# Performance work log

Measured on AMD Instinct MI355X. Metric: run time of the kernel, lower is better.

## Reference

```python
import jax, jax.numpy as jnp
import numpy as np

B, N, DIN, D, PHI, RHO, L = 4096, 10, 32, 128, 256, 128, 3
EPS = 1e-5


def setup_inputs() -> dict:
    key = jax.random.key(0)
    ks = jax.random.split(key, 24)
    def p(k, shape):
        return jax.random.normal(k, shape, jnp.float32) * 0.05
    return {
        "A": jax.random.normal(ks[0], (B, N, N), jnp.float32),
        "X": jax.random.normal(ks[1], (B, N, DIN), jnp.float32),
        "home_mask": jax.random.randint(ks[2], (B, N), 0, 2).astype(jnp.int32),
        "We1": p(ks[3], (DIN, D)), "be1": p(ks[4], (D,)),
        "We2": p(ks[5], (D, D)), "be2": p(ks[6], (D,)),
        "rgcn_w": p(ks[7], (L, 2, D, D)),      # per-relation weights
        "rgcn_root": p(ks[8], (L, D, D)),       # root (self) weight
        "rgcn_b": p(ks[9], (L, D)),
        "l1w": p(ks[10], (L, D, D)), "l1b": p(ks[11], (L, D)),
        "l2w": p(ks[12], (L, D, D)), "l2b": p(ks[13], (L, D)),
        "ln_g": jnp.ones((D,), jnp.float32), "ln_b": jnp.zeros((D,), jnp.float32),
        "p1w": p(ks[14], (D, PHI)), "p1b": p(ks[15], (PHI,)),
        "p2w": p(ks[16], (PHI, PHI)), "p2b": p(ks[17], (PHI,)),
        "r1w": p(ks[18], (PHI, RHO)), "r1b": p(ks[19], (RHO,)),
        "r2w": p(ks[20], (RHO, 1)), "r2b": p(ks[21], (1,)),
    }


def _layernorm(x, g, b):
    mu = x.mean(-1, keepdims=True)
    var = ((x - mu) ** 2).mean(-1, keepdims=True)
    return (x - mu) / jnp.sqrt(var + EPS) * g + b


def reference(A, X, home_mask, We1, be1, We2, be2, rgcn_w, rgcn_root, rgcn_b,
              l1w, l1b, l2w, l2b, ln_g, ln_b, p1w, p1b, p2w, p2b,
              r1w, r1b, r2w, r2b):
    BN = B * N
    hm = home_mask.astype(jnp.float32)
    am = 1.0 - hm
    # embedders (dropout layers are identity in eval)
    H = jax.nn.relu(X @ We1 + be1)
    H = (H @ We2 + be2).reshape(BN, D)
    # A ~ randn is nonzero everywhere -> edge list = all (b,i,j) pairs,
    # in the same row-major order torch.nonzero produces.
    bidx = jnp.repeat(jnp.arange(BN), N)          # b*N+i for each edge (row)
    row = bidx
    col = (jnp.repeat(jnp.arange(B), N * N) * N + jnp.tile(jnp.arange(N), BN))
    ew = A.reshape(-1)                             # edge weight
    aw = jnp.abs(ew)
    m1 = (ew > 0).astype(jnp.float32)              # relation 1 mask
    m0 = 1.0 - m1                                  # relation 0 mask
    agg = jnp.zeros_like(H)
    for l in range(L):
        H = H + agg
        # RGCNConv (mean aggregation per relation + root + bias)
        xj = H[row]                                # [E, D] gather of sources
        s0 = jax.ops.segment_sum(xj * m0[:, None], col, num_segments=BN)
        s1 = jax.ops.segment_sum(xj * m1[:, None], col, num_segments=BN)
        c0 = jax.ops.segment_sum(m0, col, num_segments=BN)
        c1 = jax.ops.segment_sum(m1, col, num_segments=BN)
        mean0 = s0 / jnp.maximum(c0, 1.0)[:, None]
        mean1 = s1 / jnp.maximum(c1, 1.0)[:, None]
        H2 = mean0 @ rgcn_w[l, 0] + mean1 @ rgcn_w[l, 1] + H @ rgcn_root[l] + rgcn_b[l]
        # outer gather-scale-scatter
        msg = H2[col] * aw[:, None]                # [E, D]
        agg = jax.ops.segment_sum(msg, row, num_segments=BN)
        agg = jax.nn.relu(_layernorm(agg, ln_g, ln_b))
        # Linear -> ReLU -> (Dropout=id) -> Linear
        agg = jax.nn.relu(agg @ l1w[l] + l1b[l])
        agg = agg @ l2w[l] + l2b[l]
    H = (H + agg).reshape(B, N, D)
    # DeepSet phi (dropout = identity)
    phi = jax.nn.relu(H @ p1w + p1b)
    phi = jax.nn.relu(phi @ p2w + p2b)             # [B, N, PHI]
    hs = (phi * hm[..., None]).sum(axis=1)
    aws = (phi * am[..., None]).sum(axis=1)
    def rho(s):
        return (jax.nn.relu(s @ r1w + r1b) @ r2w + r2b)[..., 0]
    return 0.5 + 0.5 * jnp.tanh(rho(hs) - rho(aws))
```

## Files before the change

kernel.cpp:

```cpp
#include <hip/hip_runtime.h>
#include <math.h>

#define B_    4096
#define N_    10
#define DIN_  32
#define D_    128
#define PHI_  256
#define RHO_  128
#define L_    3
#define EPS_  1e-5f

__device__ __forceinline__ short f2bs(float f) {
    unsigned u = __float_as_uint(f);
    u += 0x7fffu + ((u >> 16) & 1u);
    return (short)(u >> 16);
}
__device__ __forceinline__ float bs2f(short s) {
    return __uint_as_float(((unsigned)(unsigned short)s) << 16);
}

typedef short bf16x8 __attribute__((ext_vector_type(8)));
typedef float f32x4  __attribute__((ext_vector_type(4)));
typedef float v2f    __attribute__((ext_vector_type(2)));

__device__ __forceinline__ v2f splat2(float s) { v2f r; r.x = s; r.y = s; return r; }
__device__ __forceinline__ v2f fma2(v2f a, v2f b, v2f c) { return __builtin_elementwise_fma(a, b, c); }

#define WS_WE1 0
#define WS_WE2 4096
#define WS_RGW 20480
#define WS_RGR 118784
#define WS_L1  167936
#define WS_L2  217088
#define WS_P1  266240
#define WS_P2  299008
#define WS_R1  364544

__global__ __launch_bounds__(64)
void prep_weights(const float* __restrict__ We1, const float* __restrict__ We2,
                  const float* __restrict__ rgw, const float* __restrict__ rgr,
                  const float* __restrict__ l1w, const float* __restrict__ l2w,
                  const float* __restrict__ p1w, const float* __restrict__ p2w,
                  const float* __restrict__ r1w, short* __restrict__ ws)
{
    int bi = blockIdx.x, l = threadIdx.x;
    const float* src; int KS, Nw, dstOff, tt;
    if      (bi <   8) { src = We1; KS = 1; Nw = 128; dstOff = WS_WE1; tt = bi; }
    else if (bi <  40) { src = We2; KS = 4; Nw = 128; dstOff = WS_WE2; tt = bi - 8; }
    else if (bi < 232) { int m = (bi - 40) >> 5;  src = rgw + m * 16384; KS = 4; Nw = 128; dstOff = WS_RGW + m * 16384; tt = (bi - 40)  & 31; }
    else if (bi < 328) { int m = (bi - 232) >> 5; src = rgr + m * 16384; KS = 4; Nw = 128; dstOff = WS_RGR + m * 16384; tt = (bi - 232) & 31; }
    else if (bi < 424) { int m = (bi - 328) >> 5; src = l1w + m * 16384; KS = 4; Nw = 128; dstOff = WS_L1  + m * 16384; tt = (bi - 328) & 31; }
    else if (bi < 520) { int m = (bi - 424) >> 5; src = l2w + m * 16384; KS = 4; Nw = 128; dstOff = WS_L2  + m * 16384; tt = (bi - 424) & 31; }
    else if (bi < 584) { src = p1w; KS = 4; Nw = 256; dstOff = WS_P1; tt = bi - 520; }
    else if (bi < 712) { src = p2w; KS = 8; Nw = 256; dstOff = WS_P2; tt = bi - 584; }
    else               { src = r1w; KS = 8; Nw = 128; dstOff = WS_R1; tt = bi - 712; }
    int nt = tt / KS, ks = tt - nt * KS;
    int kbase = ks * 32 + (l >> 4) * 8;
    int col   = nt * 16 + (l & 15);
    union { short s[8]; int4 v; } u;
#pragma unroll
    for (int j = 0; j < 8; ++j)
        u.s[j] = f2bs(src[(size_t)(kbase + j) * Nw + col]);
    *(int4*)(ws + dstOff + ((size_t)tt * 64 + l) * 8) = u.v;
}


template<int NT>
__device__ __forceinline__ void initC(f32x4* acc, const float* __restrict__ bias, int c16) {
#pragma unroll
    for (int nt = 0; nt < NT; ++nt) {
        float bv = bias[nt * 16 + c16];
        acc[nt] = (f32x4){bv, bv, bv, bv};
    }
}

template<int KS, int NT>
__device__ __forceinline__ void mm_a16(const short* __restrict__ Wf, const short* __restrict__ Ab,
                                       int ldA, int mrow, int q, int l, f32x4* acc) {
#pragma unroll
    for (int ks = 0; ks < KS; ++ks) {
        bf16x8 a = *(const bf16x8*)(Ab + mrow * ldA + ks * 32 + q * 8);
#pragma unroll
        for (int nt = 0; nt < NT; ++nt) {
            bf16x8 bv = *(const bf16x8*)(Wf + ((size_t)(nt * KS + ks) * 64 + l) * 8);
            acc[nt] = __builtin_amdgcn_mfma_f32_16x16x32_bf16(a, bv, acc[nt], 0, 0, 0);
        }
    }
}

template<int KS, int NT>
__device__ __forceinline__ void mm_a32(const short* __restrict__ Wf, const float* __restrict__ Af,
                                       int ldA, int mrow, int q, int l, f32x4* acc) {
#pragma unroll
    for (int ks = 0; ks < KS; ++ks) {
        const float* p = Af + mrow * ldA + ks * 32 + q * 8;
        f32x4 x0 = *(const f32x4*)p;
        f32x4 x1 = *(const f32x4*)(p + 4);
        bf16x8 a;
        a[0] = f2bs(x0[0]); a[1] = f2bs(x0[1]); a[2] = f2bs(x0[2]); a[3] = f2bs(x0[3]);
        a[4] = f2bs(x1[0]); a[5] = f2bs(x1[1]); a[6] = f2bs(x1[2]); a[7] = f2bs(x1[3]);
#pragma unroll
        for (int nt = 0; nt < NT; ++nt) {
            bf16x8 bv = *(const bf16x8*)(Wf + ((size_t)(nt * KS + ks) * 64 + l) * 8);
            acc[nt] = __builtin_amdgcn_mfma_f32_16x16x32_bf16(a, bv, acc[nt], 0, 0, 0);
        }
    }
}

template<int KS>
__device__ __forceinline__ void mm8p_a16(const short* __restrict__ Wf,
                                         const short* __restrict__ Ab, int ldA,
                                         int mrow, int q, int l, f32x4* acc)
{
    const short* ap = Ab + mrow * ldA + q * 8;
    const short* wp = Wf + l * 8;
    bf16x8 acur = *(const bf16x8*)ap;
    bf16x8 bcur[8], bnxt[8];
#pragma unroll
    for (int nt = 0; nt < 8; ++nt) bcur[nt] = *(const bf16x8*)(wp + (size_t)nt * KS * 512);
#pragma unroll
    for (int ks = 0; ks < KS; ++ks) {
        bf16x8 anxt = acur;
#pragma unroll
        for (int nt = 0; nt < 8; ++nt) bnxt[nt] = bcur[nt];
        if (ks + 1 < KS) {
            anxt = *(const bf16x8*)(ap + (ks + 1) * 32);
#pragma unroll
            for (int nt = 0; nt < 8; ++nt)
                bnxt[nt] = *(const bf16x8*)(wp + (size_t)(nt * KS + ks + 1) * 512);
        }
#pragma unroll
        for (int nt = 0; nt < 8; ++nt)
            acc[nt] = __builtin_amdgcn_mfma_f32_16x16x32_bf16(acur, bcur[nt], acc[nt], 0, 0, 0);
        acur = anxt;
#pragma unroll
        for (int nt = 0; nt < 8; ++nt) bcur[nt] = bnxt[nt];
    }
}

template<int KS>
__device__ __forceinline__ void mm8p_a32(const short* __restrict__ Wf,
                                         const float* __restrict__ Af, int ldA,
                                         int mrow, int q, int l, f32x4* acc)
{
    const float* ap = Af + mrow * ldA + q * 8;
    const short* wp = Wf + l * 8;
    auto cvt = [&](int ks) {
        f32x4 x0 = *(const f32x4*)(ap + ks * 32);
        f32x4 x1 = *(const f32x4*)(ap + ks * 32 + 4);
        bf16x8 a;
        a[0] = f2bs(x0[0]); a[1] = f2bs(x0[1]); a[2] = f2bs(x0[2]); a[3] = f2bs(x0[3]);
        a[4] = f2bs(x1[0]); a[5] = f2bs(x1[1]); a[6] = f2bs(x1[2]); a[7] = f2bs(x1[3]);
        return a;
    };
    bf16x8 acur = cvt(0);
    bf16x8 bcur[8], bnxt[8];
#pragma unroll
    for (int nt = 0; nt < 8; ++nt) bcur[nt] = *(const bf16x8*)(wp + (size_t)nt * KS * 512);
#pragma unroll
    for (int ks = 0; ks < KS; ++ks) {
        bf16x8 anxt = acur;
#pragma unroll
        for (int nt = 0; nt < 8; ++nt) bnxt[nt] = bcur[nt];
        if (ks + 1 < KS) {
            anxt = cvt(ks + 1);
#pragma unroll
            for (int nt = 0; nt < 8; ++nt)
                bnxt[nt] = *(const bf16x8*)(wp + (size_t)(nt * KS + ks + 1) * 512);
        }
#pragma unroll
        for (int nt = 0; nt < 8; ++nt)
            acc[nt] = __builtin_amdgcn_mfma_f32_16x16x32_bf16(acur, bcur[nt], acc[nt], 0, 0, 0);
        acur = anxt;
#pragma unroll
        for (int nt = 0; nt < 8; ++nt) bcur[nt] = bnxt[nt];
    }
}

template<int NT, bool RELU>
__device__ __forceinline__ void storeC16(const f32x4* acc, short* __restrict__ dst,
                                         int ldD, int q, int c16) {
#pragma unroll
    for (int nt = 0; nt < NT; ++nt) {
#pragma unroll
        for (int i = 0; i < 4; ++i) {
            int r = q * 4 + i;
            if (r < 10) {
                float v = acc[nt][i];
                if (RELU) v = fmaxf(v, 0.f);
                dst[r * ldD + nt * 16 + c16] = f2bs(v);
            }
        }
    }
}

#define HLD  132
#define GLD  264
#define H2LD 136

__global__ __launch_bounds__(64, 2)
void gcn_main(const float* __restrict__ A, const float* __restrict__ X,
              const int* __restrict__ home_mask,
              const float* __restrict__ be1, const float* __restrict__ be2,
              const float* __restrict__ rgcn_b,
              const float* __restrict__ l1b, const float* __restrict__ l2b,
              const float* __restrict__ ln_g, const float* __restrict__ ln_b,
              const float* __restrict__ p1b, const float* __restrict__ p2b,
              const float* __restrict__ r1b, const float* __restrict__ r2w,
              const short* __restrict__ ws, float* __restrict__ out)
{
    const int b   = blockIdx.x;
    const int l   = threadIdx.x;
    const int q   = l >> 4;
    const int c16 = l & 15;
    const int mrow = (c16 < 10) ? c16 : 9;

    __shared__ __align__(16) float HfS[N_ * HLD];
    __shared__ __align__(16) short GbS[N_ * GLD];
    __shared__ __align__(16) short H2S[N_ * H2LD];
    __shared__ float AabsS[100], M1S[100];
    __shared__ float invc0S[N_], invc1S[N_];
    __shared__ float hmfS[16], awfS[16];

    short* S0 = GbS;
    short* S1 = GbS + 136;
    short* RhoS = H2S;

    {
        const float* Ab = A + (size_t)b * 100;
#pragma unroll
        for (int e = l; e < 100; e += 64) {
            float a = Ab[e];
            AabsS[e] = fabsf(a);
            M1S[e]  = (a > 0.f) ? 1.f : 0.f;
        }
        if (l < 16) {
            float hm = 0.f, aw = 0.f;
            if (l < 10) { hm = (float)home_mask[b * N_ + l]; aw = 1.f - hm; }
            hmfS[l] = hm; awfS[l] = aw;
        }
        if (l < 10) {
            float c1 = 0.f;
#pragma unroll
            for (int i = 0; i < 10; ++i) c1 += M1S[i * 10 + l];
            invc1S[l] = 1.f / fmaxf(c1, 1.f);
            invc0S[l] = 1.f / fmaxf(10.f - c1, 1.f);
        }
    }

    {
        f32x4 acc[8];
        initC<8>(acc, be1, c16);
        const float* xg = X + (size_t)b * (N_ * DIN_) + mrow * DIN_ + q * 8;
        f32x4 x0 = *(const f32x4*)xg;
        f32x4 x1 = *(const f32x4*)(xg + 4);
        bf16x8 a;
        a[0] = f2bs(x0[0]); a[1] = f2bs(x0[1]); a[2] = f2bs(x0[2]); a[3] = f2bs(x0[3]);
        a[4] = f2bs(x1[0]); a[5] = f2bs(x1[1]); a[6] = f2bs(x1[2]); a[7] = f2bs(x1[3]);
#pragma unroll
        for (int nt = 0; nt < 8; ++nt) {
            bf16x8 bv = *(const bf16x8*)(ws + WS_WE1 + ((size_t)nt * 64 + l) * 8);
            acc[nt] = __builtin_amdgcn_mfma_f32_16x16x32_bf16(a, bv, acc[nt], 0, 0, 0);
        }
        storeC16<8, true>(acc, S0, GLD, q, c16);
    }
    {
        f32x4 acc[8];
        initC<8>(acc, be2, c16);
        mm8p_a16<4>(ws + WS_WE2, S0, GLD, mrow, q, l, acc);
#pragma unroll
        for (int nt = 0; nt < 8; ++nt)
#pragma unroll
            for (int i = 0; i < 4; ++i) {
                int r = q * 4 + i;
                if (r < 10) HfS[r * HLD + nt * 16 + c16] = acc[nt][i];
            }
    }

    const v2f lg2 = *(const v2f*)(ln_g + 2 * l);
    const v2f lb2 = *(const v2f*)(ln_b + 2 * l);

    for (int ll = 0; ll < L_; ++ll) {
        {
            v2f hv[N_];
#pragma unroll
            for (int i = 0; i < N_; ++i) hv[i] = *(const v2f*)(HfS + i * HLD + 2 * l);
            v2f st = hv[0];
#pragma unroll
            for (int i = 1; i < N_; ++i) st += hv[i];
#pragma unroll
            for (int j = 0; j < N_; ++j) {
                v2f s1 = splat2(0.f);
#pragma unroll
                for (int i = 0; i < N_; ++i) s1 = fma2(splat2(M1S[i * 10 + j]), hv[i], s1);
                v2f m0 = (st - s1) * splat2(invc0S[j]);
                v2f m1 = s1 * splat2(invc1S[j]);
                short2 w0; w0.x = f2bs(m0.x); w0.y = f2bs(m0.y);
                short2 w1; w1.x = f2bs(m1.x); w1.y = f2bs(m1.y);
                *(short2*)(S0 + j * GLD + 2 * l) = w0;
                *(short2*)(S1 + j * GLD + 2 * l) = w1;
            }
        }
        {
            f32x4 acc[8];
            initC<8>(acc, rgcn_b + ll * D_, c16);
            mm8p_a16<4>(ws + WS_RGW + (size_t)(ll * 2 + 0) * 16384, S0, GLD, mrow, q, l, acc);
            mm8p_a16<4>(ws + WS_RGW + (size_t)(ll * 2 + 1) * 16384, S1, GLD, mrow, q, l, acc);
            mm8p_a32<4>(ws + WS_RGR + (size_t)ll * 16384, HfS, HLD, mrow, q, l, acc);
            storeC16<8, false>(acc, H2S, H2LD, q, c16);
        }
        {
            v2f ag[N_];
#pragma unroll
            for (int i = 0; i < N_; ++i) ag[i] = splat2(0.f);
#pragma unroll
            for (int j = 0; j < N_; ++j) {
                short2 hh = *(const short2*)(H2S + j * H2LD + 2 * l);
                v2f h2; h2.x = bs2f(hh.x); h2.y = bs2f(hh.y);
#pragma unroll
                for (int i = 0; i < N_; ++i)
                    ag[i] = fma2(splat2(AabsS[i * 10 + j]), h2, ag[i]);
            }
#pragma unroll
            for (int i = 0; i < N_; ++i) {
                float s  = ag[i].x + ag[i].y;
                float ss = fmaf(ag[i].x, ag[i].x, ag[i].y * ag[i].y);
#pragma unroll
                for (int off = 32; off > 0; off >>= 1) {
                    s  += __shfl_xor(s,  off);
                    ss += __shfl_xor(ss, off);
                }
                float mu   = s * (1.f / 128.f);
                float var  = ss * (1.f / 128.f) - mu * mu;
                float rstd = rsqrtf(var + EPS_);
                v2f v = fma2((ag[i] - splat2(mu)) * splat2(rstd), lg2, lb2);
                short2 wv; wv.x = f2bs(fmaxf(v.x, 0.f)); wv.y = f2bs(fmaxf(v.y, 0.f));
                *(short2*)(S0 + i * GLD + 2 * l) = wv;
            }
        }
        {
            f32x4 acc[8];
            initC<8>(acc, l1b + ll * D_, c16);
            mm8p_a16<4>(ws + WS_L1 + (size_t)ll * 16384, S0, GLD, mrow, q, l, acc);
            storeC16<8, true>(acc, S1, GLD, q, c16);
        }
        {
            f32x4 acc[8];
            initC<8>(acc, l2b + ll * D_, c16);
            mm8p_a16<4>(ws + WS_L2 + (size_t)ll * 16384, S1, GLD, mrow, q, l, acc);
#pragma unroll
            for (int nt = 0; nt < 8; ++nt)
#pragma unroll
                for (int i = 0; i < 4; ++i) {
                    int r = q * 4 + i;
                    if (r < 10) HfS[r * HLD + nt * 16 + c16] += acc[nt][i];
                }
        }
    }

    {
        f32x4 acc[16];
        initC<16>(acc, p1b, c16);
        mm_a32<4, 16>(ws + WS_P1, HfS, HLD, mrow, q, l, acc);
        storeC16<16, true>(acc, GbS, GLD, q, c16);
    }
    {
        f32x4 acc[16];
        initC<16>(acc, p2b, c16);
        mm_a16<8, 16>(ws + WS_P2, GbS, GLD, mrow, q, l, acc);
        float hm0 = hmfS[q * 4 + 0], hm1 = hmfS[q * 4 + 1], hm2 = hmfS[q * 4 + 2], hm3 = hmfS[q * 4 + 3];
        float aw0 = awfS[q * 4 + 0], aw1 = awfS[q * 4 + 1], aw2 = awfS[q * 4 + 2], aw3 = awfS[q * 4 + 3];
#pragma unroll
        for (int t = 0; t < 16; ++t) {
            float v0 = fmaxf(acc[t][0], 0.f), v1 = fmaxf(acc[t][1], 0.f);
            float v2 = fmaxf(acc[t][2], 0.f), v3 = fmaxf(acc[t][3], 0.f);
            float hp = hm0 * v0 + hm1 * v1 + hm2 * v2 + hm3 * v3;
            float ap = aw0 * v0 + aw1 * v1 + aw2 * v2 + aw3 * v3;
            hp += __shfl_xor(hp, 16); hp += __shfl_xor(hp, 32);
            ap += __shfl_xor(ap, 16); ap += __shfl_xor(ap, 32);
            if (l < 16) {
                RhoS[t * 16 + l]       = f2bs(hp);
                RhoS[256 + t * 16 + l] = f2bs(ap);
            }
        }
    }
    {
        f32x4 acc[8];
        initC<8>(acc, r1b, c16);
        const int rr = (c16 < 2) ? c16 : 0;
        mm_a16<8, 8>(ws + WS_R1, RhoS, 256, rr, q, l, acc);
        float d = 0.f;
        if (q == 0) {
#pragma unroll
            for (int t = 0; t < 8; ++t) {
                float vh = fmaxf(acc[t][0], 0.f);
                float va = fmaxf(acc[t][1], 0.f);
                d = fmaf(vh - va, r2w[t * 16 + c16], d);
            }
        }
#pragma unroll
        for (int off = 32; off > 0; off >>= 1) d += __shfl_xor(d, off);
        if (l == 0) out[b] = 0.5f + 0.5f * tanhf(d);
    }
}

extern "C" void kernel_launch(void* const* d_in, const int* in_sizes, int n_in,
                              void* d_out, int out_size, void* d_ws, size_t ws_size,
                              hipStream_t stream) {
    const float* A         = (const float*)d_in[0];
    const float* X         = (const float*)d_in[1];
    const int*   home_mask = (const int*)  d_in[2];
    const float* We1       = (const float*)d_in[3];
    const float* be1       = (const float*)d_in[4];
    const float* We2       = (const float*)d_in[5];
    const float* be2       = (const float*)d_in[6];
    const float* rgcn_w    = (const float*)d_in[7];
    const float* rgcn_root = (const float*)d_in[8];
    const float* rgcn_b    = (const float*)d_in[9];
    const float* l1w       = (const float*)d_in[10];
    const float* l1b       = (const float*)d_in[11];
    const float* l2w       = (const float*)d_in[12];
    const float* l2b       = (const float*)d_in[13];
    const float* ln_g      = (const float*)d_in[14];
    const float* ln_b      = (const float*)d_in[15];
    const float* p1w       = (const float*)d_in[16];
    const float* p1b       = (const float*)d_in[17];
    const float* p2w       = (const float*)d_in[18];
    const float* p2b       = (const float*)d_in[19];
    const float* r1w       = (const float*)d_in[20];
    const float* r1b       = (const float*)d_in[21];
    const float* r2w       = (const float*)d_in[22];

    short* ws = (short*)d_ws;

    prep_weights<<<776, 64, 0, stream>>>(We1, We2, rgcn_w, rgcn_root,
                                         l1w, l2w, p1w, p2w, r1w, ws);
    gcn_main<<<B_, 64, 0, stream>>>(A, X, home_mask, be1, be2, rgcn_b,
                                    l1b, l2b, ln_g, ln_b, p1b, p2b,
                                    r1b, r2w, ws, (float*)d_out);
}
```

Measured before the change: 253.3 us.

## Process two graphs per wavefront to reuse weight fragments across MFMAs

Each 64-thread block now handles two batch graphs instead of one, with every shared buffer duplicated. Each loaded weight fragment feeds MFMAs for both graphs, halving weight-load traffic per graph and giving more independent MFMA chains to hide latency. The phi layers are split into two 128-wide halves so the new two-accumulator routine fits in registers. The cost is roughly double the LDS and register use per block, fewer blocks in the grid, and possibly lower occupancy.

```diff
diff --git a/kernel.cpp b/kernel.cpp
--- a/kernel.cpp
+++ b/kernel.cpp
@@ -74,104 +74,87 @@
     }
 }
 
-template<int KS, int NT>
-__device__ __forceinline__ void mm_a16(const short* __restrict__ Wf, const short* __restrict__ Ab,
-                                       int ldA, int mrow, int q, int l, f32x4* acc) {
+template<int KS>
+__device__ __forceinline__ void mm8p2_a16(const short* __restrict__ Wf,
+                                          const short* __restrict__ A0,
+                                          const short* __restrict__ A1, int ldA,
+                                          int mrow, int q, int l,
+                                          f32x4* acc0, f32x4* acc1)
+{
+    const short* ap0 = A0 + mrow * ldA + q * 8;
+    const short* ap1 = A1 + mrow * ldA + q * 8;
+    const short* wp  = Wf + l * 8;
+    bf16x8 a0 = *(const bf16x8*)ap0;
+    bf16x8 a1 = *(const bf16x8*)ap1;
+    bf16x8 bcur[8], bnxt[8];
+#pragma unroll
+    for (int nt = 0; nt < 8; ++nt) bcur[nt] = *(const bf16x8*)(wp + (size_t)nt * KS * 512);
 #pragma unroll
     for (int ks = 0; ks < KS; ++ks) {
-        bf16x8 a = *(const bf16x8*)(Ab + mrow * ldA + ks * 32 + q * 8);
-#pragma unroll
-        for (int nt = 0; nt < NT; ++nt) {
-            bf16x8 bv = *(const bf16x8*)(Wf + ((size_t)(nt * KS + ks) * 64 + l) * 8);
-            acc[nt] = __builtin_amdgcn_mfma_f32_16x16x32_bf16(a, bv, acc[nt], 0, 0, 0);
-        }
-    }
-}
-
-template<int KS, int NT>
-__device__ __forceinline__ void mm_a32(const short* __restrict__ Wf, const float* __restrict__ Af,
-                                       int ldA, int mrow, int q, int l, f32x4* acc) {
-#pragma unroll
-    for (int ks = 0; ks < KS; ++ks) {
-        const float* p = Af + mrow * ldA + ks * 32 + q * 8;
+        bf16x8 a0n = a0, a1n = a1;
+#pragma unroll
+        for (int nt = 0; nt < 8; ++nt) bnxt[nt] = bcur[nt];
+        if (ks + 1 < KS) {
+            a0n = *(const bf16x8*)(ap0 + (ks + 1) * 32);
+            a1n = *(const bf16x8*)(ap1 + (ks + 1) * 32);
+#pragma unroll
+            for (int nt = 0; nt < 8; ++nt)
+                bnxt[nt] = *(const bf16x8*)(wp + (size_t)(nt * KS + ks + 1) * 512);
+        }
+#pragma unroll
+        for (int nt = 0; nt < 8; ++nt)
+            acc0[nt] = __builtin_amdgcn_mfma_f32_16x16x32_bf16(a0, bcur[nt], acc0[nt], 0, 0, 0);
+#pragma unroll
+        for (int nt = 0; nt < 8; ++nt)
+            acc1[nt] = __builtin_amdgcn_mfma_f32_16x16x32_bf16(a1, bcur[nt], acc1[nt], 0, 0, 0);
+        a0 = a0n; a1 = a1n;
+#pragma unroll
+        for (int nt = 0; nt < 8; ++nt) bcur[nt] = bnxt[nt];
+    }
+}
+
+template<int KS>
+__device__ __forceinline__ void mm8p2_a32(const short* __restrict__ Wf,
+                                          const float* __restrict__ A0,
+                                          const float* __restrict__ A1, int ldA,
+                                          int mrow, int q, int l,
+                                          f32x4* acc0, f32x4* acc1)
+{
+    const float* ap0 = A0 + mrow * ldA + q * 8;
+    const float* ap1 = A1 + mrow * ldA + q * 8;
+    const short* wp  = Wf + l * 8;
+    auto cvt = [](const float* p) {
         f32x4 x0 = *(const f32x4*)p;
         f32x4 x1 = *(const f32x4*)(p + 4);
         bf16x8 a;
         a[0] = f2bs(x0[0]); a[1] = f2bs(x0[1]); a[2] = f2bs(x0[2]); a[3] = f2bs(x0[3]);
         a[4] = f2bs(x1[0]); a[5] = f2bs(x1[1]); a[6] = f2bs(x1[2]); a[7] = f2bs(x1[3]);
-#pragma unroll
-        for (int nt = 0; nt < NT; ++nt) {
-            bf16x8 bv = *(const bf16x8*)(Wf + ((size_t)(nt * KS + ks) * 64 + l) * 8);
-            acc[nt] = __builtin_amdgcn_mfma_f32_16x16x32_bf16(a, bv, acc[nt], 0, 0, 0);
-        }
-    }
-}
-
-template<int KS>
-__device__ __forceinline__ void mm8p_a16(const short* __restrict__ Wf,
-                                         const short* __restrict__ Ab, int ldA,
-                                         int mrow, int q, int l, f32x4* acc)
-{
-    const short* ap = Ab + mrow * ldA + q * 8;
-    const short* wp = Wf + l * 8;
-    bf16x8 acur = *(const bf16x8*)ap;
+        return a;
+    };
+    bf16x8 a0 = cvt(ap0);
+    bf16x8 a1 = cvt(ap1);
     bf16x8 bcur[8], bnxt[8];
 #pragma unroll
     for (int nt = 0; nt < 8; ++nt) bcur[nt] = *(const bf16x8*)(wp + (size_t)nt * KS * 512);
 #pragma unroll
     for (int ks = 0; ks < KS; ++ks) {
-        bf16x8 anxt = acur;
+        bf16x8 a0n = a0, a1n = a1;
 #pragma unroll
         for (int nt = 0; nt < 8; ++nt) bnxt[nt] = bcur[nt];
         if (ks + 1 < KS) {
-            anxt = *(const bf16x8*)(ap + (ks + 1) * 32);
+            a0n = cvt(ap0 + (ks + 1) * 32);
+            a1n = cvt(ap1 + (ks + 1) * 32);
 #pragma unroll
             for (int nt = 0; nt < 8; ++nt)
                 bnxt[nt] = *(const bf16x8*)(wp + (size_t)(nt * KS + ks + 1) * 512);
         }
 #pragma unroll
         for (int nt = 0; nt < 8; ++nt)
-            acc[nt] = __builtin_amdgcn_mfma_f32_16x16x32_bf16(acur, bcur[nt], acc[nt], 0, 0, 0);
-        acur = anxt;
-#pragma unroll
-        for (int nt = 0; nt < 8; ++nt) bcur[nt] = bnxt[nt];
-    }
-}
-
-template<int KS>
-__device__ __forceinline__ void mm8p_a32(const short* __restrict__ Wf,
-                                         const float* __restrict__ Af, int ldA,
-                                         int mrow, int q, int l, f32x4* acc)
-{
-    const float* ap = Af + mrow * ldA + q * 8;
-    const short* wp = Wf + l * 8;
-    auto cvt = [&](int ks) {
-        f32x4 x0 = *(const f32x4*)(ap + ks * 32);
-        f32x4 x1 = *(const f32x4*)(ap + ks * 32 + 4);
-        bf16x8 a;
-        a[0] = f2bs(x0[0]); a[1] = f2bs(x0[1]); a[2] = f2bs(x0[2]); a[3] = f2bs(x0[3]);
-        a[4] = f2bs(x1[0]); a[5] = f2bs(x1[1]); a[6] = f2bs(x1[2]); a[7] = f2bs(x1[3]);
-        return a;
-    };
-    bf16x8 acur = cvt(0);
-    bf16x8 bcur[8], bnxt[8];
-#pragma unroll
-    for (int nt = 0; nt < 8; ++nt) bcur[nt] = *(const bf16x8*)(wp + (size_t)nt * KS * 512);
-#pragma unroll
-    for (int ks = 0; ks < KS; ++ks) {
-        bf16x8 anxt = acur;
-#pragma unroll
-        for (int nt = 0; nt < 8; ++nt) bnxt[nt] = bcur[nt];
-        if (ks + 1 < KS) {
-            anxt = cvt(ks + 1);
-#pragma unroll
-            for (int nt = 0; nt < 8; ++nt)
-                bnxt[nt] = *(const bf16x8*)(wp + (size_t)(nt * KS + ks + 1) * 512);
-        }
+            acc0[nt] = __builtin_amdgcn_mfma_f32_16x16x32_bf16(a0, bcur[nt], acc0[nt], 0, 0, 0);
 #pragma unroll
         for (int nt = 0; nt < 8; ++nt)
-            acc[nt] = __builtin_amdgcn_mfma_f32_16x16x32_bf16(acur, bcur[nt], acc[nt], 0, 0, 0);
-        acur = anxt;
+            acc1[nt] = __builtin_amdgcn_mfma_f32_16x16x32_bf16(a1, bcur[nt], acc1[nt], 0, 0, 0);
+        a0 = a0n; a1 = a1n;
 #pragma unroll
         for (int nt = 0; nt < 8; ++nt) bcur[nt] = bnxt[nt];
     }
@@ -209,71 +192,85 @@
               const float* __restrict__ r1b, const float* __restrict__ r2w,
               const short* __restrict__ ws, float* __restrict__ out)
 {
-    const int b   = blockIdx.x;
+    const int b0  = blockIdx.x * 2;
     const int l   = threadIdx.x;
     const int q   = l >> 4;
     const int c16 = l & 15;
     const int mrow = (c16 < 10) ? c16 : 9;
 
-    __shared__ __align__(16) float HfS[N_ * HLD];
-    __shared__ __align__(16) short GbS[N_ * GLD];
-    __shared__ __align__(16) short H2S[N_ * H2LD];
-    __shared__ float AabsS[100], M1S[100];
-    __shared__ float invc0S[N_], invc1S[N_];
-    __shared__ float hmfS[16], awfS[16];
-
-    short* S0 = GbS;
-    short* S1 = GbS + 136;
-    short* RhoS = H2S;
-
-    {
-        const float* Ab = A + (size_t)b * 100;
-#pragma unroll
-        for (int e = l; e < 100; e += 64) {
-            float a = Ab[e];
-            AabsS[e] = fabsf(a);
-            M1S[e]  = (a > 0.f) ? 1.f : 0.f;
+    __shared__ __align__(16) float HfS[2][N_ * HLD];
+    __shared__ __align__(16) short GbS[2][N_ * GLD];
+    __shared__ __align__(16) short H2S[2][N_ * H2LD];
+    __shared__ float AabsS[2][100], M1S[2][100];
+    __shared__ float invc0S[2][N_], invc1S[2][N_];
+    __shared__ float hmfS[2][16], awfS[2][16];
+
+    {
+#pragma unroll
+        for (int e = l; e < 200; e += 64) {
+            int g = (e >= 100) ? 1 : 0;
+            int e2 = e - g * 100;
+            float a = A[(size_t)(b0 + g) * 100 + e2];
+            AabsS[g][e2] = fabsf(a);
+            M1S[g][e2]  = (a > 0.f) ? 1.f : 0.f;
         }
         if (l < 16) {
-            float hm = 0.f, aw = 0.f;
-            if (l < 10) { hm = (float)home_mask[b * N_ + l]; aw = 1.f - hm; }
-            hmfS[l] = hm; awfS[l] = aw;
+#pragma unroll
+            for (int g = 0; g < 2; ++g) {
+                float hm = 0.f, aw = 0.f;
+                if (l < 10) { hm = (float)home_mask[(b0 + g) * N_ + l]; aw = 1.f - hm; }
+                hmfS[g][l] = hm; awfS[g][l] = aw;
+            }
         }
         if (l < 10) {
-            float c1 = 0.f;
-#pragma unroll
-            for (int i = 0; i < 10; ++i) c1 += M1S[i * 10 + l];
-            invc1S[l] = 1.f / fmaxf(c1, 1.f);
-            invc0S[l] = 1.f / fmaxf(10.f - c1, 1.f);
-        }
-    }
-
-    {
-        f32x4 acc[8];
-        initC<8>(acc, be1, c16);
-        const float* xg = X + (size_t)b * (N_ * DIN_) + mrow * DIN_ + q * 8;
-        f32x4 x0 = *(const f32x4*)xg;
-        f32x4 x1 = *(const f32x4*)(xg + 4);
-        bf16x8 a;
-        a[0] = f2bs(x0[0]); a[1] = f2bs(x0[1]); a[2] = f2bs(x0[2]); a[3] = f2bs(x0[3]);
-        a[4] = f2bs(x1[0]); a[5] = f2bs(x1[1]); a[6] = f2bs(x1[2]); a[7] = f2bs(x1[3]);
+#pragma unroll
+            for (int g = 0; g < 2; ++g) {
+                float c1 = 0.f;
+#pragma unroll
+                for (int i = 0; i < 10; ++i) c1 += M1S[g][i * 10 + l];
+                invc1S[g][l] = 1.f / fmaxf(c1, 1.f);
+                invc0S[g][l] = 1.f / fmaxf(10.f - c1, 1.f);
+            }
+        }
+    }
+
+    {
+        f32x4 acc0[8], acc1[8];
+        initC<8>(acc0, be1, c16);
+        initC<8>(acc1, be1, c16);
+        auto cvtX = [&](int g) {
+            const float* xg = X + (size_t)(b0 + g) * (N_ * DIN_) + mrow * DIN_ + q * 8;
+            f32x4 x0 = *(const f32x4*)xg;
+            f32x4 x1 = *(const f32x4*)(xg + 4);
+            bf16x8 a;
+            a[0] = f2bs(x0[0]); a[1] = f2bs(x0[1]); a[2] = f2bs(x0[2]); a[3] = f2bs(x0[3]);
+            a[4] = f2bs(x1[0]); a[5] = f2bs(x1[1]); a[6] = f2bs(x1[2]); a[7] = f2bs(x1[3]);
+            return a;
+        };
+        bf16x8 a0 = cvtX(0), a1 = cvtX(1);
 #pragma unroll
         for (int nt = 0; nt < 8; ++nt) {
             bf16x8 bv = *(const bf16x8*)(ws + WS_WE1 + ((size_t)nt * 64 + l) * 8);
-            acc[nt] = __builtin_amdgcn_mfma_f32_16x16x32_bf16(a, bv, acc[nt], 0, 0, 0);
-        }
-        storeC16<8, true>(acc, S0, GLD, q, c16);
-    }
-    {
-        f32x4 acc[8];
-        initC<8>(acc, be2, c16);
-        mm8p_a16<4>(ws + WS_WE2, S0, GLD, mrow, q, l, acc);
+            acc0[nt] = __builtin_amdgcn_mfma_f32_16x16x32_bf16(a0, bv, acc0[nt], 0, 0, 0);
+            acc1[nt] = __builtin_amdgcn_mfma_f32_16x16x32_bf16(a1, bv, acc1[nt], 0, 0, 0);
+        }
+        storeC16<8, true>(acc0, &GbS[0][0], GLD, q, c16);
+        storeC16<8, true>(acc1, &GbS[1][0], GLD, q, c16);
+    }
+    {
+        f32x4 acc0[8], acc1[8];
+        initC<8>(acc0, be2, c16);
+        initC<8>(acc1, be2, c16);
+        mm8p2_a16<4>(ws + WS_WE2, &GbS[0][0], &GbS[1][0], GLD, mrow, q, l, acc0, acc1);
 #pragma unroll
         for (int nt = 0; nt < 8; ++nt)
 #pragma unroll
             for (int i = 0; i < 4; ++i) {
                 int r = q * 4 + i;
-                if (r < 10) HfS[r * HLD + nt * 16 + c16] = acc[nt][i];
+                if (r < 10) {
+                    HfS[0][r * HLD + nt * 16 + c16] = acc0[nt][i];
+                    HfS[1][r * HLD + nt * 16 + c16] = acc1[nt][i];
+                }
             }
     }
 
@@ -281,10 +278,11 @@
     const v2f lb2 = *(const v2f*)(ln_b + 2 * l);
 
     for (int ll = 0; ll < L_; ++ll) {
-        {
+#pragma unroll
+        for (int g = 0; g < 2; ++g) {
             v2f hv[N_];
 #pragma unroll
-            for (int i = 0; i < N_; ++i) hv[i] = *(const v2f*)(HfS + i * HLD + 2 * l);
+            for (int i = 0; i < N_; ++i) hv[i] = *(const v2f*)(&HfS[g][i * HLD] + 2 * l);
             v2f st = hv[0];
 #pragma unroll
             for (int i = 1; i < N_; ++i) st += hv[i];
@@ -292,34 +290,40 @@
             for (int j = 0; j < N_; ++j) {
                 v2f s1 = splat2(0.f);
 #pragma unroll
-                for (int i = 0; i < N_; ++i) s1 = fma2(splat2(M1S[i * 10 + j]), hv[i], s1);
-                v2f m0 = (st - s1) * splat2(invc0S[j]);
-                v2f m1 = s1 * splat2(invc1S[j]);
+                for (int i = 0; i < N_; ++i) s1 = fma2(splat2(M1S[g][i * 10 + j]), hv[i], s1);
+                v2f m0 = (st - s1) * splat2(invc0S[g][j]);
+                v2f m1 = s1 * splat2(invc1S[g][j]);
                 short2 w0; w0.x = f2bs(m0.x); w0.y = f2bs(m0.y);
                 short2 w1; w1.x = f2bs(m1.x); w1.y = f2bs(m1.y);
-                *(short2*)(S0 + j * GLD + 2 * l) = w0;
-                *(short2*)(S1 + j * GLD + 2 * l) = w1;
+                *(short2*)(&GbS[g][j * GLD]       + 2 * l) = w0;
+                *(short2*)(&GbS[g][j * GLD + 136] + 2 * l) = w1;
             }
         }
         {
-            f32x4 acc[8];
-            initC<8>(acc, rgcn_b + ll * D_, c16);
-            mm8p_a16<4>(ws + WS_RGW + (size_t)(ll * 2 + 0) * 16384, S0, GLD, mrow, q, l, acc);
-            mm8p_a16<4>(ws + WS_RGW + (size_t)(ll * 2 + 1) * 16384, S1, GLD, mrow, q, l, acc);
-            mm8p_a32<4>(ws + WS_RGR + (size_t)ll * 16384, HfS, HLD, mrow, q, l, acc);
-            storeC16<8, false>(acc, H2S, H2LD, q, c16);
-        }
-        {
+            f32x4 acc0[8], acc1[8];
+            initC<8>(acc0, rgcn_b + ll * D_, c16);
+            initC<8>(acc1, rgcn_b + ll * D_, c16);
+            mm8p2_a16<4>(ws + WS_RGW + (size_t)(ll * 2 + 0) * 16384,
+                         &GbS[0][0],   &GbS[1][0],   GLD, mrow, q, l, acc0, acc1);
+            mm8p2_a16<4>(ws + WS_RGW + (size_t)(ll * 2 + 1) * 16384,
+                         &GbS[0][136], &GbS[1][136], GLD, mrow, q, l, acc0, acc1);
+            mm8p2_a32<4>(ws + WS_RGR + (size_t)ll * 16384,
+                         &HfS[0][0], &HfS[1][0], HLD, mrow, q, l, acc0, acc1);
+            storeC16<8, false>(acc0, &H2S[0][0], H2LD, q, c16);
+            storeC16<8, false>(acc1, &H2S[1][0], H2LD, q, c16);
+        }
+#pragma unroll
+        for (int g = 0; g < 2; ++g) {
             v2f ag[N_];
 #pragma unroll
             for (int i = 0; i < N_; ++i) ag[i] = splat2(0.f);
 #pragma unroll
             for (int j = 0; j < N_; ++j) {
-                short2 hh = *(const short2*)(H2S + j * H2LD + 2 * l);
+                short2 hh = *(const short2*)(&H2S[g][j * H2LD] + 2 * l);
                 v2f h2; h2.x = bs2f(hh.x); h2.y = bs2f(hh.y);
 #pragma unroll
                 for (int i = 0; i < N_; ++i)
-                    ag[i] = fma2(splat2(AabsS[i * 10 + j]), h2, ag[i]);
+                    ag[i] = fma2(splat2(AabsS[g][i * 10 + j]), h2, ag[i]);
             }
 #pragma unroll
             for (int i = 0; i < N_; ++i) {
@@ -335,72 +339,105 @@
                 float rstd = rsqrtf(var + EPS_);
                 v2f v = fma2((ag[i] - splat2(mu)) * splat2(rstd), lg2, lb2);
                 short2 wv; wv.x = f2bs(fmaxf(v.x, 0.f)); wv.y = f2bs(fmaxf(v.y, 0.f));
-                *(short2*)(S0 + i * GLD + 2 * l) = wv;
+                *(short2*)(&GbS[g][i * GLD] + 2 * l) = wv;
             }
         }
         {
-            f32x4 acc[8];
-            initC<8>(acc, l1b + ll * D_, c16);
-            mm8p_a16<4>(ws + WS_L1 + (size_t)ll * 16384, S0, GLD, mrow, q, l, acc);
-            storeC16<8, true>(acc, S1, GLD, q, c16);
+            f32x4 acc0[8], acc1[8];
+            initC<8>(acc0, l1b + ll * D_, c16);
+            initC<8>(acc1, l1b + ll * D_, c16);
+            mm8p2_a16<4>(ws + WS_L1 + (size_t)ll * 16384,
+                         &GbS[0][0], &GbS[1][0], GLD, mrow, q, l, acc0, acc1);
+            storeC16<8, true>(acc0, &GbS[0][136], GLD, q, c16);
+            storeC16<8, true>(acc1, &GbS[1][136], GLD, q, c16);
         }
         {
-            f32x4 acc[8];
-            initC<8>(acc, l2b + ll * D_, c16);
-            mm8p_a16<4>(ws + WS_L2 + (size_t)ll * 16384, S1, GLD, mrow, q, l, acc);
+            f32x4 acc0[8], acc1[8];
+            initC<8>(acc0, l2b + ll * D_, c16);
+            initC<8>(acc1, l2b + ll * D_, c16);
+            mm8p2_a16<4>(ws + WS_L2 + (size_t)ll * 16384,
+                         &GbS[0][136], &GbS[1][136], GLD, mrow, q, l, acc0, acc1);
 #pragma unroll
             for (int nt = 0; nt < 8; ++nt)
 #pragma unroll
                 for (int i = 0; i < 4; ++i) {
                     int r = q * 4 + i;
-                    if (r < 10) HfS[r * HLD + nt * 16 + c16] += acc[nt][i];
+                    if (r < 10) {
+                        HfS[0][r * HLD + nt * 16 + c16] += acc0[nt][i];
+                        HfS[1][r * HLD + nt * 16 + c16] += acc1[nt][i];
+                    }
                 }
         }
     }
 
     {
-        f32x4 acc[16];
-        initC<16>(acc, p1b, c16);
-        mm_a32<4, 16>(ws + WS_P1, HfS, HLD, mrow, q, l, acc);
-        storeC16<16, true>(acc, GbS, GLD, q, c16);
-    }
-    {
-        f32x4 acc[16];
-        initC<16>(acc, p2b, c16);
-        mm_a16<8, 16>(ws + WS_P2, GbS, GLD, mrow, q, l, acc);
-        float hm0 = hmfS[q * 4 + 0], hm1 = hmfS[q * 4 + 1], hm2 = hmfS[q * 4 + 2], hm3 = hmfS[q * 4 + 3];
-        float aw0 = awfS[q * 4 + 0], aw1 = awfS[q * 4 + 1], aw2 = awfS[q * 4 + 2], aw3 = awfS[q * 4 + 3];
-#pragma unroll
-        for (int t = 0; t < 16; ++t) {
-            float v0 = fmaxf(acc[t][0], 0.f), v1 = fmaxf(acc[t][1], 0.f);
-            float v2 = fmaxf(acc[t][2], 0.f), v3 = fmaxf(acc[t][3], 0.f);
-            float hp = hm0 * v0 + hm1 * v1 + hm2 * v2 + hm3 * v3;
-            float ap = aw0 * v0 + aw1 * v1 + aw2 * v2 + aw3 * v3;
-            hp += __shfl_xor(hp, 16); hp += __shfl_xor(hp, 32);
-            ap += __shfl_xor(ap, 16); ap += __shfl_xor(ap, 32);
-            if (l < 16) {
-                RhoS[t * 16 + l]       = f2bs(hp);
-                RhoS[256 + t * 16 + l] = f2bs(ap);
-            }
-        }
-    }
-    {
-        f32x4 acc[8];
-        initC<8>(acc, r1b, c16);
+        f32x4 acc0[8], acc1[8];
+        initC<8>(acc0, p1b, c16);
+        initC<8>(acc1, p1b, c16);
+        mm8p2_a32<4>(ws + WS_P1, &HfS[0][0], &HfS[1][0], HLD, mrow, q, l, acc0, acc1);
+        storeC16<8, true>(acc0, &GbS[0][0], GLD, q, c16);
+        storeC16<8, true>(acc1, &GbS[1][0], GLD, q, c16);
+        initC<8>(acc0, p1b + 128, c16);
+        initC<8>(acc1, p1b + 128, c16);
+        mm8p2_a32<4>(ws + WS_P1 + 8 * 4 * 512, &HfS[0][0], &HfS[1][0], HLD, mrow, q, l, acc0, acc1);
+        storeC16<8, true>(acc0, &GbS[0][128], GLD, q, c16);
+        storeC16<8, true>(acc1, &GbS[1][128], GLD, q, c16);
+    }
+    {
+#pragma unroll
+        for (int half = 0; half < 2; ++half) {
+            f32x4 acc0[8], acc1[8];
+            initC<8>(acc0, p2b + half * 128, c16);
+            initC<8>(acc1, p2b + half * 128, c16);
+            mm8p2_a16<8>(ws + WS_P2 + (size_t)half * 8 * 8 * 512,
+                         &GbS[0][0], &GbS[1][0], GLD, mrow, q, l, acc0, acc1);
+#pragma unroll
+            for (int g = 0; g < 2; ++g) {
+                const f32x4* acc = (g == 0) ? acc0 : acc1;
+                float hm0 = hmfS[g][q * 4 + 0], hm1 = hmfS[g][q * 4 + 1];
+                float hm2 = hmfS[g][q * 4 + 2], hm3 = hmfS[g][q * 4 + 3];
+                float aw0 = awfS[g][q * 4 + 0], aw1 = awfS[g][q * 4 + 1];
+                float aw2 = awfS[g][q * 4 + 2], aw3 = awfS[g][q * 4 + 3];
+#pragma unroll
+                for (int t = 0; t < 8; ++t) {
+                    float v0 = fmaxf(acc[t][0], 0.f), v1 = fmaxf(acc[t][1], 0.f);
+                    float v2 = fmaxf(acc[t][2], 0.f), v3 = fmaxf(acc[t][3], 0.f);
+                    float hp = hm0 * v0 + hm1 * v1 + hm2 * v2 + hm3 * v3;
+                    float ap = aw0 * v0 + aw1 * v1 + aw2 * v2 + aw3 * v3;
+                    hp += __shfl_xor(hp, 16); hp += __shfl_xor(hp, 32);
+                    ap += __shfl_xor(ap, 16); ap += __shfl_xor(ap, 32);
+                    if (l < 16) {
+                        H2S[g][(half * 8 + t) * 16 + l]       = f2bs(hp);
+                        H2S[g][256 + (half * 8 + t) * 16 + l] = f2bs(ap);
+                    }
+                }
+            }
+        }
+    }
+    {
+        f32x4 acc0[8], acc1[8];
+        initC<8>(acc0, r1b, c16);
+        initC<8>(acc1, r1b, c16);
         const int rr = (c16 < 2) ? c16 : 0;
-        mm_a16<8, 8>(ws + WS_R1, RhoS, 256, rr, q, l, acc);
-        float d = 0.f;
+        mm8p2_a16<8>(ws + WS_R1, &H2S[0][0], &H2S[1][0], 256, rr, q, l, acc0, acc1);
+        float d0 = 0.f, d1 = 0.f;
         if (q == 0) {
 #pragma unroll
             for (int t = 0; t < 8; ++t) {
-                float vh = fmaxf(acc[t][0], 0.f);
-                float va = fmaxf(acc[t][1], 0.f);
-                d = fmaf(vh - va, r2w[t * 16 + c16], d);
-            }
-        }
-#pragma unroll
-        for (int off = 32; off > 0; off >>= 1) d += __shfl_xor(d, off);
-        if (l == 0) out[b] = 0.5f + 0.5f * tanhf(d);
+                float w = r2w[t * 16 + c16];
+                d0 = fmaf(fmaxf(acc0[t][0], 0.f) - fmaxf(acc0[t][1], 0.f), w, d0);
+                d1 = fmaf(fmaxf(acc1[t][0], 0.f) - fmaxf(acc1[t][1], 0.f), w, d1);
+            }
+        }
+#pragma unroll
+        for (int off = 32; off > 0; off >>= 1) {
+            d0 += __shfl_xor(d0, off);
+            d1 += __shfl_xor(d1, off);
+        }
+        if (l == 0) {
+            out[b0]     = 0.5f + 0.5f * tanhf(d0);
+            out[b0 + 1] = 0.5f + 0.5f * tanhf(d1);
+        }
     }
 }
 
@@ -435,7 +472,7 @@
 
     prep_weights<<<776, 64, 0, stream>>>(We1, We2, rgcn_w, rgcn_root,
                                          l1w, l2w, p1w, p2w, r1w, ws);
-    gcn_main<<<B_, 64, 0, stream>>>(A, X, home_mask, be1, be2, rgcn_b,
-                                    l1b, l2b, ln_g, ln_b, p1b, p2b,
-                                    r1b, r2w, ws, (float*)d_out);
-}
+    gcn_main<<<B_ / 2, 64, 0, stream>>>(A, X, home_mask, be1, be2, rgcn_b,
+                                        l1b, l2b, ln_g, ln_b, p1b, p2b,
+                                        r1b, r2w, ws, (float*)d_out);
+}
```

After: 269.1 us. 1.06x slower.
